# Optimization experiments

Hardware: AMD Instinct MI355X
Metric: run time of the kernel (lower is better)

Reference implementation:

```python
import jax, jax.numpy as jnp
import numpy as np

EPS_DIST = 1e-10
BN_EPS = 1e-5
K = 3  # nsample / three_nn


def setup_inputs() -> dict:
    key = jax.random.key(0)
    ks = jax.random.split(key, 8)
    B, N, S, D1, D2 = 4, 8192, 2048, 128, 256
    C_in = D1 + D2  # 384
    H = 256
    inp = {
        "pos1": jax.random.normal(ks[0], (B, 3, N), dtype=jnp.float32),
        "pos2": jax.random.normal(ks[1], (B, 3, S), dtype=jnp.float32),
        "feature1": jax.random.normal(ks[2], (B, D1, N), dtype=jnp.float32),
        "feature2": jax.random.normal(ks[3], (B, D2, S), dtype=jnp.float32),
        # MLP layer 1: Conv1d(384->256, k=1) + BN
        "W1": jax.random.normal(ks[4], (H, C_in), dtype=jnp.float32) * (1.0 / np.sqrt(C_in)),
        "b1": jnp.zeros((H,), dtype=jnp.float32),
        "g1": jnp.ones((H,), dtype=jnp.float32),
        "be1": jnp.zeros((H,), dtype=jnp.float32),
        # MLP layer 2: Conv1d(256->256, k=1) + BN
        "W2": jax.random.normal(ks[5], (H, H), dtype=jnp.float32) * (1.0 / np.sqrt(H)),
        "b2": jnp.zeros((H,), dtype=jnp.float32),
        "g2": jnp.ones((H,), dtype=jnp.float32),
        "be2": jnp.zeros((H,), dtype=jnp.float32),
    }
    return inp


def _conv_bn_relu(x, W, b, gamma, beta):
    # x: [B, Cin, N]; 1x1 Conv1d == channel GEMM
    y = jnp.einsum("oc,bcn->bon", W, x) + b[None, :, None]
    # BatchNorm1d in training mode: batch statistics over (B, N)
    mean = jnp.mean(y, axis=(0, 2), keepdims=True)
    var = jnp.mean(jnp.square(y - mean), axis=(0, 2), keepdims=True)
    y = (y - mean) * jax.lax.rsqrt(var + BN_EPS)
    y = y * gamma[None, :, None] + beta[None, :, None]
    return jax.nn.relu(y)


def reference(pos1, pos2, feature1, feature2, W1, b1, g1, be1, W2, b2, g2, be2):
    # pos1: [B,3,N], pos2: [B,3,S], feature1: [B,D1,N], feature2: [B,D2,S]
    p1 = jnp.swapaxes(pos1, 1, 2)  # [B,N,3]
    p2 = jnp.swapaxes(pos2, 1, 2)  # [B,S,3]
    # three_nn: squared-distance 3-NN of each point in p1 among p2
    d2 = (jnp.sum(p1 * p1, -1)[:, :, None]
          + jnp.sum(p2 * p2, -1)[:, None, :]
          - 2.0 * jnp.einsum("bnc,bsc->bns", p1, p2))  # [B,N,S]
    neg_vals, idx = jax.lax.top_k(-d2, K)  # idx: [B,N,3]
    dists = jnp.maximum(-neg_vals, EPS_DIST)  # dists[dists<1e-10]=1e-10
    w = 1.0 / dists
    w = w / jnp.sum(w, -1, keepdims=True)  # [B,N,3]
    # grouping_operation: gather feature2 [B,D,S] by idx -> [B,D,N,3]
    grouped = jax.vmap(lambda f, i: f[:, i])(feature2, idx)
    interpolated = jnp.sum(grouped * w[:, None, :, :], axis=-1)  # [B,D2,N]
    feat = jnp.concatenate([interpolated, feature1], axis=1)  # [B,384,N]
    feat = _conv_bn_relu(feat, W1, b1, g1, be1)
    feat = _conv_bn_relu(feat, W2, b2, g2, be2)
    return feat  # [B,256,N]
```

## Files before the change

kernel.cpp:

```cpp
#include <hip/hip_runtime.h>
#include <hip/hip_bf16.h>
#include <cstdint>

typedef unsigned short u16;
typedef unsigned int u32;
typedef unsigned long long u64;
typedef __bf16 bf16x8 __attribute__((ext_vector_type(8)));
typedef float f32x4 __attribute__((ext_vector_type(4)));
typedef u16 u16x8 __attribute__((ext_vector_type(8)));

#define FPSCALE 1048576.0f
#define FPINV   (1.0f / 1048576.0f)
#define NSLICE 16

__device__ __forceinline__ u16 f2b(float f) {
    unsigned int u = __float_as_uint(f);
    u += 0x7fffu + ((u >> 16) & 1u);
    return (u16)(u >> 16);
}
__device__ __forceinline__ float b2f(u16 h) {
    return __uint_as_float(((unsigned int)h) << 16);
}
__device__ __forceinline__ void async_cp16(void* lds, const void* g) {
    __builtin_amdgcn_global_load_lds((const __attribute__((address_space(1))) void*)g,
                                     (__attribute__((address_space(3))) void*)lds, 16, 0, 0);
}
__device__ __forceinline__ u64 ld_agent_u64(const u64* p) {
    return __hip_atomic_load(p, __ATOMIC_RELAXED, __HIP_MEMORY_SCOPE_AGENT);
}
__device__ __forceinline__ u32 fmono(float f) {
    u32 u = __float_as_uint(f);
    return u ^ (((u32)((int)u >> 31)) | 0x80000000u);
}
__device__ __forceinline__ u64 shfl_xor_u64(u64 v, int mask) {
    u32 lo = (u32)v, hi = (u32)(v >> 32);
    lo = (u32)__shfl_xor((int)lo, mask);
    hi = (u32)__shfl_xor((int)hi, mask);
    return ((u64)hi << 32) | lo;
}
__device__ __forceinline__ void ins3(u64 k, u64& k0, u64& k1, u64& k2) {
    bool c0 = k > k0, c1 = k > k1, c2 = k > k2;
    k2 = c1 ? k1 : (c2 ? k : k2);
    k1 = c0 ? k0 : (c1 ? k : k1);
    k0 = c0 ? k : k0;
}
__device__ __forceinline__ int pkix(int i) { return i + (i >> 6); }

#define NB_NN  2048
#define NB_CVT 160
#define NB_T2  512
#define NB_T1  1024

__global__ __launch_bounds__(256, 8) void prep_kernel(const float* __restrict__ w1,
                                                      const float* __restrict__ w2,
                                                      u16* __restrict__ wb,
                                                      const float* __restrict__ feature2,
                                                      u16* __restrict__ f2t,
                                                      const float* __restrict__ feature1,
                                                      u16* __restrict__ f1t,
                                                      const float* __restrict__ pos1,
                                                      const float* __restrict__ pos2,
                                                      int* __restrict__ idx_out,
                                                      float* __restrict__ w_out,
                                                      u64* __restrict__ SZ) {
    __shared__ __align__(16) char smem[18176];
    int bi = blockIdx.x;
    int tid = threadIdx.x;

    if (bi >= NB_NN) {
        int ci = bi - NB_NN;
        if (ci >= NB_CVT + NB_T2 + NB_T1) {
            for (int i = tid; i < 2 * NSLICE * 512; i += 256) SZ[i] = 0;
            if (tid == 0) *(int*)(SZ + 2 * NSLICE * 512) = 0;
            return;
        }
        if (ci < NB_CVT) {
            int i = ci * 256 + tid;
            if (i < 40960) {
                const float* src = (i < 24576) ? w1 : w2;
                int k = (i < 24576) ? i : (i - 24576);
                float4 v = *(const float4*)&src[(size_t)k * 4];
                ushort4 o;
                o.x = f2b(v.x); o.y = f2b(v.y); o.z = f2b(v.z); o.w = f2b(v.w);
                *(ushort4*)&wb[(size_t)i * 4] = o;
            }
            return;
        }
        float (*t)[65] = (float (*)[65])smem;
        const float* in; u16* out; int C, S, s0, c0, b;
        if (ci < NB_CVT + NB_T2) {
            int lin = ci - NB_CVT;
            C = 256; S = 2048; in = feature2; out = f2t;
            s0 = (lin & 31) * 64; c0 = ((lin >> 5) & 3) * 64; b = lin >> 7;
        } else {
            int lin = ci - NB_CVT - NB_T2;
            C = 128; S = 8192; in = feature1; out = f1t;
            s0 = (lin & 127) * 64; c0 = ((lin >> 7) & 1) * 64; b = lin >> 8;
        }
        const float* ib = in + (size_t)b * C * S;
        u16* ob = out + (size_t)b * S * C;
        int col = tid & 63, r0 = tid >> 6;
#pragma unroll
        for (int p = 0; p < 16; ++p) {
            int c = p * 4 + r0;
            t[c][col] = ib[(size_t)(c0 + c) * S + s0 + col];
        }
        __syncthreads();
#pragma unroll
        for (int p = 0; p < 16; ++p) {
            int s = p * 4 + r0;
            ob[(size_t)(s0 + s) * C + c0 + col] = f2b(t[col][s]);
        }
        return;
    }

    float4* pk = (float4*)smem;
    u64* warr = (u64*)(smem + 16640);
    int j0 = bi * 16;
    int b = j0 >> 13;
    const float* p2 = pos2 + (size_t)b * 3 * 2048;
    int p = tid & 15, ck = tid >> 4;
    int wv = tid >> 6, lane = tid & 63;
    const float* p1 = pos1 + (size_t)b * 3 * 8192;
    int n = (j0 & 8191) + p;
    float qx = p1[n], qy = p1[8192 + n], qz = p1[16384 + n];
    u64 key0 = 0, key1 = 0, key2 = 0;

    for (int half = 0; half < 2; ++half) {
        int hbase = half * 1024;
        for (int i = tid; i < 1024; i += 256) {
            int s = hbase + i;
            float x = p2[s], y = p2[2048 + s], z = p2[4096 + s];
            pk[pkix(i)] = make_float4(x, y, z, -0.5f * (x * x + y * y + z * z));
        }
        __syncthreads();

        float g0 = -3.4e38f, g1 = -3.4e38f, g2 = -3.4e38f;
        int id0 = 0, id1 = 0, id2 = 0;
        int sb = ck * 64;
        const float4* pc = pk + pkix(sb);
#pragma unroll 4
        for (int it = 0; it < 64; ++it) {
            float4 cd = pc[it];
            int s = sb + it;
            float tv = fmaf(qx, cd.x, fmaf(qy, cd.y, fmaf(qz, cd.z, cd.w)));
            bool c0 = tv > g0, c1 = tv > g1, c2 = tv > g2;
            float o0 = g0, o1 = g1;
            g2 = __builtin_amdgcn_fmed3f(tv, o1, g2);
            g1 = __builtin_amdgcn_fmed3f(tv, o0, o1);
            g0 = fmaxf(o0, tv);
            id2 = c1 ? id1 : (c2 ? s : id2);
            id1 = c0 ? id0 : (c1 ? s : id1);
            id0 = c0 ? s : id0;
        }
        __syncthreads();

        ins3(((u64)fmono(g0) << 32) | (u64)(2047 - (hbase + id0)), key0, key1, key2);
        ins3(((u64)fmono(g1) << 32) | (u64)(2047 - (hbase + id1)), key0, key1, key2);
        ins3(((u64)fmono(g2) << 32) | (u64)(2047 - (hbase + id2)), key0, key1, key2);
    }

#pragma unroll
    for (int mask = 16; mask <= 32; mask <<= 1) {
        u64 m0 = shfl_xor_u64(key0, mask);
        u64 m1 = shfl_xor_u64(key1, mask);
        u64 m2 = shfl_xor_u64(key2, mask);
        ins3(m0, key0, key1, key2);
        ins3(m1, key0, key1, key2);
        ins3(m2, key0, key1, key2);
    }
    if (lane < 16) {
        u64* wr = &warr[(wv * 16 + p) * 3];
        wr[0] = key0; wr[1] = key1; wr[2] = key2;
    }
    __syncthreads();
    if (tid < 16) {
        int pp = tid;
        const u64* w0 = &warr[pp * 3];
        u64 k0 = w0[0], k1 = w0[1], k2 = w0[2];
#pragma unroll
        for (int w = 1; w < 4; ++w) {
            const u64* wr = &warr[(w * 16 + pp) * 3];
            ins3(wr[0], k0, k1, k2);
            ins3(wr[1], k0, k1, k2);
            ins3(wr[2], k0, k1, k2);
        }
        int s0 = 2047 - (int)(k0 & 0xFFFFFFFFu);
        int s1 = 2047 - (int)(k1 & 0xFFFFFFFFu);
        int s2 = 2047 - (int)(k2 & 0xFFFFFFFFu);
        int j = j0 + pp;
        int nn = j & 8191;
        float x1 = p1[nn], y1 = p1[8192 + nn], z1 = p1[16384 + nn];
        float n1 = x1 * x1 + y1 * y1 + z1 * z1;
        float X0 = p2[s0], Y0 = p2[2048 + s0], Z0 = p2[4096 + s0];
        float X1 = p2[s1], Y1v = p2[2048 + s1], Z1 = p2[4096 + s1];
        float X2 = p2[s2], Y2v = p2[2048 + s2], Z2 = p2[4096 + s2];
        float t0 = x1 * X0 + y1 * Y0 + z1 * Z0 - 0.5f * (X0 * X0 + Y0 * Y0 + Z0 * Z0);
        float t1 = x1 * X1 + y1 * Y1v + z1 * Z1 - 0.5f * (X1 * X1 + Y1v * Y1v + Z1 * Z1);
        float t2 = x1 * X2 + y1 * Y2v + z1 * Z2 - 0.5f * (X2 * X2 + Y2v * Y2v + Z2 * Z2);
        float d0 = fmaxf(fmaf(-2.f, t0, n1), 1e-10f);
        float d1 = fmaxf(fmaf(-2.f, t1, n1), 1e-10f);
        float d2 = fmaxf(fmaf(-2.f, t2, n1), 1e-10f);
        float w0v = 1.f / d0, w1v = 1.f / d1, w2v = 1.f / d2;
        float inv = 1.f / (w0v + w1v + w2v);
        idx_out[j * 3] = s0; idx_out[j * 3 + 1] = s1; idx_out[j * 3 + 2] = s2;
        w_out[j * 3] = w0v * inv; w_out[j * 3 + 1] = w1v * inv; w_out[j * 3 + 2] = w2v * inv;
    }
}

__global__ __launch_bounds__(256, 8) void interp_kernel(const u16* __restrict__ f2t,
                                                        const int* __restrict__ idx,
                                                        const float* __restrict__ wgt,
                                                        u16* __restrict__ out) {
    int tid = threadIdx.x;
    int j = blockIdx.x * 16 + (tid >> 4);
    int c0 = (tid & 15) * 16;
    int b = j >> 13;
    const u16* fb = f2t + (size_t)b * 2048 * 256;
    const u16* r0 = fb + (size_t)idx[j * 3 + 0] * 256 + c0;
    const u16* r1 = fb + (size_t)idx[j * 3 + 1] * 256 + c0;
    const u16* r2 = fb + (size_t)idx[j * 3 + 2] * 256 + c0;
    float w0 = wgt[j * 3 + 0], w1 = wgt[j * 3 + 1], w2 = wgt[j * 3 + 2];
    u16* ob = out + (size_t)j * 256 + c0;
#pragma unroll
    for (int cc = 0; cc < 2; ++cc) {
        u16x8 v0 = *(const u16x8*)(r0 + cc * 8);
        u16x8 v1 = *(const u16x8*)(r1 + cc * 8);
        u16x8 v2 = *(const u16x8*)(r2 + cc * 8);
        u16x8 o;
#pragma unroll
        for (int e = 0; e < 8; ++e)
            o[e] = f2b(w0 * b2f(v0[e]) + w1 * b2f(v1[e]) + w2 * b2f(v2[e]));
        *(u16x8*)(ob + cc * 8) = o;
    }
}

__device__ __forceinline__ void gridbar(int* cnt, int target) {
    __syncthreads();
    if (threadIdx.x == 0) {
        __hip_atomic_fetch_add(cnt, 1, __ATOMIC_RELAXED, __HIP_MEMORY_SCOPE_AGENT);
        while (__hip_atomic_load(cnt, __ATOMIC_RELAXED, __HIP_MEMORY_SCOPE_AGENT) < target)
            __builtin_amdgcn_s_sleep(16);
        __atomic_signal_fence(__ATOMIC_SEQ_CST);
    }
    __syncthreads();
}

__global__ __launch_bounds__(512, 1) void mlp_fused(const u16* __restrict__ A1,
                                                    const u16* __restrict__ A2g,
                                                    const u16* __restrict__ W1b,
                                                    const float* __restrict__ b1,
                                                    const u16* __restrict__ W2b,
                                                    const float* __restrict__ b2,
                                                    u64* __restrict__ S1,
                                                    const float* __restrict__ g1,
                                                    const float* __restrict__ be1,
                                                    u64* __restrict__ S2,
                                                    const float* __restrict__ g2,
                                                    const float* __restrict__ be2,
                                                    float* __restrict__ OUT,
                                                    int* __restrict__ BAR) {
    __shared__ __align__(16) char smem[141312];
    u16* AS  = (u16*)smem;
    u16* BS  = (u16*)(smem + 32768);
    u16* A2  = (u16*)smem;
    u16* BS2 = (u16*)(smem + 65536);
    float* SC  = (float*)(smem + 131072);
    float* SC2 = (float*)(smem + 135168);
    float2* BNT = (float2*)(smem + 139264);

    int tid = threadIdx.x, bid = blockIdx.x;
    int lane = tid & 63, wv = tid >> 6;
    int l15 = lane & 15, q = lane >> 4;
    int lrow = lane >> 3, lchunk = lane & 7, schunk = lchunk ^ lrow;
    int j0 = bid * 128;
    int rw = wv & 3;
    int cg = wv >> 2;
    int wrow = rw * 32;
    int cbase = cg * 128;
    int sl = (bid & (NSLICE - 1)) * 512;

    f32x4 acc[2][8];
#pragma unroll
    for (int i = 0; i < 2; ++i)
#pragma unroll
        for (int jj = 0; jj < 8; ++jj) acc[i][jj] = (f32x4){0.f, 0.f, 0.f, 0.f};

    auto stageB1 = [&](int buf, int k0) {
#pragma unroll
        for (int qq = 0; qq < 4; ++qq) {
            int row = wv * 32 + qq * 8;
            async_cp16(&BS[buf * 16384 + row * 64],
                       W1b + (size_t)(row + lrow) * 384 + k0 + schunk * 8);
        }
    };
    auto stageA1 = [&](int buf, int k0) {
        const u16* src; int str;
        if (k0 < 256) { src = A1 + (size_t)j0 * 256 + k0;          str = 256; }
        else          { src = A2g + (size_t)j0 * 128 + (k0 - 256); str = 128; }
#pragma unroll
        for (int qq = 0; qq < 2; ++qq) {
            int row = wv * 16 + qq * 8;
            async_cp16(&AS[buf * 8192 + row * 64],
                       src + (size_t)(row + lrow) * str + schunk * 8);
        }
    };
    auto stageB2 = [&](int buf, int k0) {
#pragma unroll
        for (int qq = 0; qq < 4; ++qq) {
            int row = wv * 32 + qq * 8;
            async_cp16(&BS2[buf * 16384 + row * 64],
                       W2b + (size_t)(row + lrow) * 256 + k0 + schunk * 8);
        }
    };

    stageB1(0, 0); stageA1(0, 0);
    __syncthreads();
    for (int t = 0; t < 6; ++t) {
        int cur = t & 1;
        if (t < 5) { stageB1(cur ^ 1, (t + 1) * 64); stageA1(cur ^ 1, (t + 1) * 64); }
#pragma unroll
        for (int ks = 0; ks < 2; ++ks) {
            bf16x8 af[2];
#pragma unroll
            for (int i = 0; i < 2; ++i) {
                int row = wrow + i * 16 + l15;
                af[i] = *(const bf16x8*)&AS[cur * 8192 + row * 64 +
                                            ((ks * 4 + q) ^ (l15 & 7)) * 8];
            }
#pragma unroll
            for (int jj = 0; jj < 8; ++jj) {
                int brow = cbase + jj * 16 + l15;
                bf16x8 bfr = *(const bf16x8*)&BS[cur * 16384 + brow * 64 +
                                                 ((ks * 4 + q) ^ (l15 & 7)) * 8];
#pragma unroll
                for (int i = 0; i < 2; ++i)
                    acc[i][jj] = __builtin_amdgcn_mfma_f32_16x16x32_bf16(af[i], bfr,
                                                                         acc[i][jj], 0, 0, 0);
            }
        }
        __syncthreads();
    }

    stageB2(0, 0);

#pragma unroll
    for (int jj = 0; jj < 8; ++jj) {
        int c = cbase + jj * 16 + l15;
        float bv = b1[c];
        float s = 0.f, s2 = 0.f;
#pragma unroll
        for (int i = 0; i < 2; ++i)
#pragma unroll
            for (int r = 0; r < 4; ++r) {
                acc[i][jj][r] += bv;
                float v = acc[i][jj][r];
                s += v; s2 += v * v;
            }
        s += __shfl_xor(s, 16); s += __shfl_xor(s, 32);
        s2 += __shfl_xor(s2, 16); s2 += __shfl_xor(s2, 32);
        if (q == 0) { SC[rw * 256 + c] = s; SC2[rw * 256 + c] = s2; }
    }
    __syncthreads();
    if (tid < 256) {
        float fs = SC[tid] + SC[256 + tid] + SC[512 + tid] + SC[768 + tid];
        float fs2 = SC2[tid] + SC2[256 + tid] + SC2[512 + tid] + SC2[768 + tid];
        atomicAdd(&S1[sl + tid], (u64)(long long)llrintf(fs * FPSCALE));
        atomicAdd(&S1[sl + 256 + tid], (u64)(long long)llrintf(fs2 * FPSCALE));
    }
    gridbar(BAR, 256);

    if (tid < 256) {
        long long su = 0, sq = 0;
#pragma unroll
        for (int r = 0; r < NSLICE; ++r) {
            su += (long long)ld_agent_u64(&S1[r * 512 + tid]);
            sq += (long long)ld_agent_u64(&S1[r * 512 + 256 + tid]);
        }
        float fs = (float)su * FPINV;
        float fs2 = (float)sq * FPINV;
        const float inv = 1.f / 32768.f;
        float mean = fs * inv;
        float var = fs2 * inv - mean * mean;
        float a = g1[tid] * rsqrtf(var + 1e-5f);
        BNT[tid] = make_float2(a, be1[tid] - mean * a);
    }
    __syncthreads();

#pragma unroll
    for (int jj = 0; jj < 8; ++jj) {
        int c = cbase + jj * 16 + l15;
        float2 bn = BNT[c];
        int chunkbase = c >> 3;
        int win = c & 7;
#pragma unroll
        for (int i = 0; i < 2; ++i)
#pragma unroll
            for (int r = 0; r < 4; ++r) {
                int row = wrow + i * 16 + q * 4 + r;
                float vb = b2f(f2b(acc[i][jj][r]));
                u16 h = f2b(fmaxf(vb * bn.x + bn.y, 0.f));
                A2[row * 256 + ((chunkbase ^ (row & 7)) * 8 + win)] = h;
            }
    }
    __syncthreads();

#pragma unroll
    for (int i = 0; i < 2; ++i)
#pragma unroll
        for (int jj = 0; jj < 8; ++jj) acc[i][jj] = (f32x4){0.f, 0.f, 0.f, 0.f};

    for (int t = 0; t < 4; ++t) {
        int cur = t & 1;
        if (t < 3) stageB2(cur ^ 1, (t + 1) * 64);
#pragma unroll
        for (int ks = 0; ks < 2; ++ks) {
            bf16x8 af[2];
            int kc = t * 8 + ks * 4 + q;
#pragma unroll
            for (int i = 0; i < 2; ++i) {
                int row = wrow + i * 16 + l15;
                af[i] = *(const bf16x8*)&A2[row * 256 + ((kc ^ (l15 & 7)) * 8)];
            }
#pragma unroll
            for (int jj = 0; jj < 8; ++jj) {
                int brow = cbase + jj * 16 + l15;
                bf16x8 bfr = *(const bf16x8*)&BS2[cur * 16384 + brow * 64 +
                                                  ((ks * 4 + q) ^ (l15 & 7)) * 8];
#pragma unroll
                for (int i = 0; i < 2; ++i)
                    acc[i][jj] = __builtin_amdgcn_mfma_f32_16x16x32_bf16(af[i], bfr,
                                                                         acc[i][jj], 0, 0, 0);
            }
        }
        __syncthreads();
    }

#pragma unroll
    for (int jj = 0; jj < 8; ++jj) {
        int c = cbase + jj * 16 + l15;
        float bv = b2[c];
        float s = 0.f, s2 = 0.f;
#pragma unroll
        for (int i = 0; i < 2; ++i)
#pragma unroll
            for (int r = 0; r < 4; ++r) {
                acc[i][jj][r] += bv;
                float v = acc[i][jj][r];
                s += v; s2 += v * v;
            }
        s += __shfl_xor(s, 16); s += __shfl_xor(s, 32);
        s2 += __shfl_xor(s2, 16); s2 += __shfl_xor(s2, 32);
        if (q == 0) { SC[rw * 256 + c] = s; SC2[rw * 256 + c] = s2; }
    }
    __syncthreads();
    if (tid < 256) {
        float fs = SC[tid] + SC[256 + tid] + SC[512 + tid] + SC[768 + tid];
        float fs2 = SC2[tid] + SC2[256 + tid] + SC2[512 + tid] + SC2[768 + tid];
        atomicAdd(&S2[sl + tid], (u64)(long long)llrintf(fs * FPSCALE));
        atomicAdd(&S2[sl + 256 + tid], (u64)(long long)llrintf(fs2 * FPSCALE));
    }
    gridbar(BAR, 512);

    if (tid < 256) {
        long long su = 0, sq = 0;
#pragma unroll
        for (int r = 0; r < NSLICE; ++r) {
            su += (long long)ld_agent_u64(&S2[r * 512 + tid]);
            sq += (long long)ld_agent_u64(&S2[r * 512 + 256 + tid]);
        }
        float fs = (float)su * FPINV;
        float fs2 = (float)sq * FPINV;
        const float inv = 1.f / 32768.f;
        float mean = fs * inv;
        float var = fs2 * inv - mean * mean;
        float a = g2[tid] * rsqrtf(var + 1e-5f);
        BNT[tid] = make_float2(a, be2[tid] - mean * a);
    }
    __syncthreads();

    int bb = j0 >> 13, nbase = j0 & 8191;
#pragma unroll
    for (int jj = 0; jj < 8; ++jj) {
        int o = cbase + jj * 16 + l15;
        float2 bn = BNT[o];
#pragma unroll
        for (int i = 0; i < 2; ++i) {
            int n0 = nbase + wrow + i * 16 + q * 4;
            float4 v;
            v.x = fmaxf(b2f(f2b(acc[i][jj][0])) * bn.x + bn.y, 0.f);
            v.y = fmaxf(b2f(f2b(acc[i][jj][1])) * bn.x + bn.y, 0.f);
            v.z = fmaxf(b2f(f2b(acc[i][jj][2])) * bn.x + bn.y, 0.f);
            v.w = fmaxf(b2f(f2b(acc[i][jj][3])) * bn.x + bn.y, 0.f);
            *(float4*)&OUT[(size_t)bb * 2097152 + (size_t)o * 8192 + n0] = v;
        }
    }
}

extern "C" void kernel_launch(void* const* d_in, const int* in_sizes, int n_in,
                              void* d_out, int out_size, void* d_ws, size_t ws_size,
                              hipStream_t stream) {
    const float* pos1 = (const float*)d_in[0];
    const float* pos2 = (const float*)d_in[1];
    const float* feature1 = (const float*)d_in[2];
    const float* feature2 = (const float*)d_in[3];
    const float* W1 = (const float*)d_in[4];
    const float* b1 = (const float*)d_in[5];
    const float* g1 = (const float*)d_in[6];
    const float* be1 = (const float*)d_in[7];
    const float* W2 = (const float*)d_in[8];
    const float* b2 = (const float*)d_in[9];
    const float* g2 = (const float*)d_in[10];
    const float* be2 = (const float*)d_in[11];

    char* ws = (char*)d_ws;
    int*    IDX   = (int*)(ws + 0);
    float*  WGT   = (float*)(ws + 393216);
    u16*    W1B   = (u16*)(ws + 786432);
    u16*    W2B   = (u16*)(ws + 983040);
    u16*    F2T   = (u16*)(ws + 1118208);
    u16*    F1T   = (u16*)(ws + 5312512);
    u16*    INTERP= (u16*)(ws + 30478336);
    u64*    SSTAT = (u64*)(ws + 47255552);
    u64*    S1    = SSTAT;
    u64*    S2    = SSTAT + NSLICE * 512;
    int*    BAR   = (int*)(SSTAT + 2 * NSLICE * 512);
    float*  OUT   = (float*)d_out;

    prep_kernel<<<NB_NN + NB_CVT + NB_T2 + NB_T1 + 1, 256, 0, stream>>>(
        W1, W2, W1B, feature2, F2T, feature1, F1T, pos1, pos2, IDX, WGT, SSTAT);
    interp_kernel<<<2048, 256, 0, stream>>>(F2T, IDX, WGT, INTERP);
    mlp_fused<<<256, 512, 0, stream>>>(INTERP, F1T, W1B, b1, W2B, b2,
                                       S1, g1, be1, S2, g2, be2, OUT, BAR);
}
```

Measured before the change: 171.5 us.

## Fuse interpolation gather into MLP GEMM A-staging and split top-3 scan into two chains

Removes the separate interp kernel. The fused MLP kernel now gathers the three neighbour rows of bf16 feature2 per point, forms the weighted sum in registers, and writes the result straight into the LDS A tile for the first three K steps. The global gather is issued before the MFMA work and written to LDS after it, so its latency can overlap compute. This avoids the round trip of the interpolated tensor through global memory and one kernel launch, at the cost of extra registers and uncoalesced gathers inside the GEMM kernel. The 3-NN scan also keeps two independent top-3 chains to break the serial dependency, then merges them.

```diff
diff --git a/kernel.cpp b/kernel.cpp
--- a/kernel.cpp
+++ b/kernel.cpp
@@ -135,29 +135,48 @@
         }
         __syncthreads();
 
-        float g0 = -3.4e38f, g1 = -3.4e38f, g2 = -3.4e38f;
-        int id0 = 0, id1 = 0, id2 = 0;
+        float ga0 = -3.4e38f, ga1 = -3.4e38f, ga2 = -3.4e38f;
+        float gb0 = -3.4e38f, gb1 = -3.4e38f, gb2 = -3.4e38f;
+        int ia0 = 0, ia1 = 0, ia2 = 0, ib0 = 0, ib1 = 0, ib2 = 0;
         int sb = ck * 64;
         const float4* pc = pk + pkix(sb);
 #pragma unroll 4
-        for (int it = 0; it < 64; ++it) {
-            float4 cd = pc[it];
-            int s = sb + it;
-            float tv = fmaf(qx, cd.x, fmaf(qy, cd.y, fmaf(qz, cd.z, cd.w)));
-            bool c0 = tv > g0, c1 = tv > g1, c2 = tv > g2;
-            float o0 = g0, o1 = g1;
-            g2 = __builtin_amdgcn_fmed3f(tv, o1, g2);
-            g1 = __builtin_amdgcn_fmed3f(tv, o0, o1);
-            g0 = fmaxf(o0, tv);
-            id2 = c1 ? id1 : (c2 ? s : id2);
-            id1 = c0 ? id0 : (c1 ? s : id1);
-            id0 = c0 ? s : id0;
+        for (int it = 0; it < 64; it += 2) {
+            float4 cdA = pc[it];
+            float4 cdB = pc[it + 1];
+            {
+                int s = sb + it;
+                float tv = fmaf(qx, cdA.x, fmaf(qy, cdA.y, fmaf(qz, cdA.z, cdA.w)));
+                bool c0 = tv > ga0, c1 = tv > ga1, c2 = tv > ga2;
+                float o0 = ga0, o1 = ga1;
+                ga2 = __builtin_amdgcn_fmed3f(tv, o1, ga2);
+                ga1 = __builtin_amdgcn_fmed3f(tv, o0, o1);
+                ga0 = fmaxf(o0, tv);
+                ia2 = c1 ? ia1 : (c2 ? s : ia2);
+                ia1 = c0 ? ia0 : (c1 ? s : ia1);
+                ia0 = c0 ? s : ia0;
+            }
+            {
+                int s = sb + it + 1;
+                float tv = fmaf(qx, cdB.x, fmaf(qy, cdB.y, fmaf(qz, cdB.z, cdB.w)));
+                bool c0 = tv > gb0, c1 = tv > gb1, c2 = tv > gb2;
+                float o0 = gb0, o1 = gb1;
+                gb2 = __builtin_amdgcn_fmed3f(tv, o1, gb2);
+                gb1 = __builtin_amdgcn_fmed3f(tv, o0, o1);
+                gb0 = fmaxf(o0, tv);
+                ib2 = c1 ? ib1 : (c2 ? s : ib2);
+                ib1 = c0 ? ib0 : (c1 ? s : ib1);
+                ib0 = c0 ? s : ib0;
+            }
         }
         __syncthreads();
 
-        ins3(((u64)fmono(g0) << 32) | (u64)(2047 - (hbase + id0)), key0, key1, key2);
-        ins3(((u64)fmono(g1) << 32) | (u64)(2047 - (hbase + id1)), key0, key1, key2);
-        ins3(((u64)fmono(g2) << 32) | (u64)(2047 - (hbase + id2)), key0, key1, key2);
+        ins3(((u64)fmono(ga0) << 32) | (u64)(2047 - (hbase + ia0)), key0, key1, key2);
+        ins3(((u64)fmono(ga1) << 32) | (u64)(2047 - (hbase + ia1)), key0, key1, key2);
+        ins3(((u64)fmono(ga2) << 32) | (u64)(2047 - (hbase + ia2)), key0, key1, key2);
+        ins3(((u64)fmono(gb0) << 32) | (u64)(2047 - (hbase + ib0)), key0, key1, key2);
+        ins3(((u64)fmono(gb1) << 32) | (u64)(2047 - (hbase + ib1)), key0, key1, key2);
+        ins3(((u64)fmono(gb2) << 32) | (u64)(2047 - (hbase + ib2)), key0, key1, key2);
     }
 
 #pragma unroll
@@ -208,33 +227,6 @@
     }
 }
 
-__global__ __launch_bounds__(256, 8) void interp_kernel(const u16* __restrict__ f2t,
-                                                        const int* __restrict__ idx,
-                                                        const float* __restrict__ wgt,
-                                                        u16* __restrict__ out) {
-    int tid = threadIdx.x;
-    int j = blockIdx.x * 16 + (tid >> 4);
-    int c0 = (tid & 15) * 16;
-    int b = j >> 13;
-    const u16* fb = f2t + (size_t)b * 2048 * 256;
-    const u16* r0 = fb + (size_t)idx[j * 3 + 0] * 256 + c0;
-    const u16* r1 = fb + (size_t)idx[j * 3 + 1] * 256 + c0;
-    const u16* r2 = fb + (size_t)idx[j * 3 + 2] * 256 + c0;
-    float w0 = wgt[j * 3 + 0], w1 = wgt[j * 3 + 1], w2 = wgt[j * 3 + 2];
-    u16* ob = out + (size_t)j * 256 + c0;
-#pragma unroll
-    for (int cc = 0; cc < 2; ++cc) {
-        u16x8 v0 = *(const u16x8*)(r0 + cc * 8);
-        u16x8 v1 = *(const u16x8*)(r1 + cc * 8);
-        u16x8 v2 = *(const u16x8*)(r2 + cc * 8);
-        u16x8 o;
-#pragma unroll
-        for (int e = 0; e < 8; ++e)
-            o[e] = f2b(w0 * b2f(v0[e]) + w1 * b2f(v1[e]) + w2 * b2f(v2[e]));
-        *(u16x8*)(ob + cc * 8) = o;
-    }
-}
-
 __device__ __forceinline__ void gridbar(int* cnt, int target) {
     __syncthreads();
     if (threadIdx.x == 0) {
@@ -246,7 +238,9 @@
     __syncthreads();
 }
 
-__global__ __launch_bounds__(512, 1) void mlp_fused(const u16* __restrict__ A1,
+__global__ __launch_bounds__(512, 1) void mlp_fused(const u16* __restrict__ F2T,
+                                                    const int* __restrict__ idx,
+                                                    const float* __restrict__ wgt,
                                                     const u16* __restrict__ A2g,
                                                     const u16* __restrict__ W1b,
                                                     const float* __restrict__ b1,
@@ -280,6 +274,21 @@
     int cbase = cg * 128;
     int sl = (bid & (NSLICE - 1)) * 512;
 
+    const u16* gp0[2]; const u16* gp1[2]; const u16* gp2[2];
+    float gw0[2], gw1[2], gw2[2];
+#pragma unroll
+    for (int qq = 0; qq < 2; ++qq) {
+        int r = wv * 16 + qq * 8 + lrow;
+        int j = j0 + r;
+        int bb = j >> 13;
+        const u16* fb = F2T + (size_t)bb * 2048 * 256;
+        gp0[qq] = fb + (size_t)idx[j * 3 + 0] * 256;
+        gp1[qq] = fb + (size_t)idx[j * 3 + 1] * 256;
+        gp2[qq] = fb + (size_t)idx[j * 3 + 2] * 256;
+        gw0[qq] = wgt[j * 3 + 0]; gw1[qq] = wgt[j * 3 + 1]; gw2[qq] = wgt[j * 3 + 2];
+    }
+    u16x8 G0[2], G1[2], G2[2];
+
     f32x4 acc[2][8];
 #pragma unroll
     for (int i = 0; i < 2; ++i)
@@ -294,15 +303,34 @@
                        W1b + (size_t)(row + lrow) * 384 + k0 + schunk * 8);
         }
     };
-    auto stageA1 = [&](int buf, int k0) {
-        const u16* src; int str;
-        if (k0 < 256) { src = A1 + (size_t)j0 * 256 + k0;          str = 256; }
-        else          { src = A2g + (size_t)j0 * 128 + (k0 - 256); str = 128; }
+    auto stageA1f1 = [&](int buf, int k0) {
+        const u16* src = A2g + (size_t)j0 * 128 + (k0 - 256);
 #pragma unroll
         for (int qq = 0; qq < 2; ++qq) {
             int row = wv * 16 + qq * 8;
             async_cp16(&AS[buf * 8192 + row * 64],
-                       src + (size_t)(row + lrow) * str + schunk * 8);
+                       src + (size_t)(row + lrow) * 128 + schunk * 8);
+        }
+    };
+    auto gissue = [&](int k0) {
+        int c = k0 + lchunk * 8;
+#pragma unroll
+        for (int qq = 0; qq < 2; ++qq) {
+            G0[qq] = *(const u16x8*)(gp0[qq] + c);
+            G1[qq] = *(const u16x8*)(gp1[qq] + c);
+            G2[qq] = *(const u16x8*)(gp2[qq] + c);
+        }
+    };
+    auto gwrite = [&](int buf) {
+#pragma unroll
+        for (int qq = 0; qq < 2; ++qq) {
+            int row = wv * 16 + qq * 8;
+            u16x8 o;
+#pragma unroll
+            for (int e = 0; e < 8; ++e)
+                o[e] = f2b(gw0[qq] * b2f(G0[qq][e]) + gw1[qq] * b2f(G1[qq][e]) +
+                           gw2[qq] * b2f(G2[qq][e]));
+            *(u16x8*)&AS[buf * 8192 + (row + lrow) * 64 + schunk * 8] = o;
         }
     };
     auto stageB2 = [&](int buf, int k0) {
@@ -314,11 +342,14 @@
         }
     };
 
-    stageB1(0, 0); stageA1(0, 0);
+    gissue(0);
+    stageB1(0, 0);
+    gwrite(0);
     __syncthreads();
     for (int t = 0; t < 6; ++t) {
         int cur = t & 1;
-        if (t < 5) { stageB1(cur ^ 1, (t + 1) * 64); stageA1(cur ^ 1, (t + 1) * 64); }
+        if (t < 3) { gissue((t + 1) * 64); stageB1(cur ^ 1, (t + 1) * 64); }
+        else if (t < 5) { stageB1(cur ^ 1, (t + 1) * 64); stageA1f1(cur ^ 1, (t + 1) * 64); }
 #pragma unroll
         for (int ks = 0; ks < 2; ++ks) {
             bf16x8 af[2];
@@ -339,6 +370,7 @@
                                                                          acc[i][jj], 0, 0, 0);
             }
         }
+        if (t < 3) gwrite(cur ^ 1);
         __syncthreads();
     }
 
@@ -520,7 +552,6 @@
     u16*    W2B   = (u16*)(ws + 983040);
     u16*    F2T   = (u16*)(ws + 1118208);
     u16*    F1T   = (u16*)(ws + 5312512);
-    u16*    INTERP= (u16*)(ws + 30478336);
     u64*    SSTAT = (u64*)(ws + 47255552);
     u64*    S1    = SSTAT;
     u64*    S2    = SSTAT + NSLICE * 512;
@@ -529,7 +560,6 @@
 
     prep_kernel<<<NB_NN + NB_CVT + NB_T2 + NB_T1 + 1, 256, 0, stream>>>(
         W1, W2, W1B, feature2, F2T, feature1, F1T, pos1, pos2, IDX, WGT, SSTAT);
-    interp_kernel<<<2048, 256, 0, stream>>>(F2T, IDX, WGT, INTERP);
-    mlp_fused<<<256, 512, 0, stream>>>(INTERP, F1T, W1B, b1, W2B, b2,
+    mlp_fused<<<256, 512, 0, stream>>>(F2T, IDX, WGT, F1T, W1B, b1, W2B, b2,
                                        S1, g1, be1, S2, g2, be2, OUT, BAR);
 }
```

Measured after the change: 169.4 us. About the same (-1.2%).
